# Performance work log

Measured on AMD Instinct MI355X. Metric: run time of the kernel, lower is better.

## Reference

```python
import jax, jax.numpy as jnp
import numpy as np

B, S, HD, NH, AH, F = 64, 256, 512, 8, 256, 2
DH = HD // NH          # item/pos head dim = 64
DA = AH // NH          # attribute head dim = 32
EPS = 1e-12


def setup_inputs() -> dict:
    key = jax.random.key(0)
    ks = iter(jax.random.split(key, 32))
    rn = lambda shape, s=1.0: jax.random.normal(next(ks), shape, dtype=jnp.float32) * s
    w = 0.02
    return {
        "input_tensor": rn((B, S, HD)),
        "attribute_table": rn((B, S, 1, AH)),
        "position_embedding": rn((B, S, HD)),
        "Wq": rn((HD, HD), w), "bq": jnp.zeros((HD,), jnp.float32),
        "Wk": rn((HD, HD), w), "bk": jnp.zeros((HD,), jnp.float32),
        "Wv": rn((HD, HD), w), "bv": jnp.zeros((HD,), jnp.float32),
        "Wqp": rn((HD, HD), w), "bqp": jnp.zeros((HD,), jnp.float32),
        "Wkp": rn((HD, HD), w), "bkp": jnp.zeros((HD,), jnp.float32),
        "Wqa": rn((F, AH, AH), w), "bqa": jnp.zeros((F, AH), jnp.float32),
        "Wka": rn((F, AH, AH), w), "bka": jnp.zeros((F, AH), jnp.float32),
        "fw1": rn((S, S), w), "fb1": jnp.zeros((S,), jnp.float32),
        "fw2": rn((1, S), w), "fb2": jnp.zeros((1,), jnp.float32),
        "Wd": rn((HD, HD), w), "bd": jnp.zeros((HD,), jnp.float32),
        "gamma": jnp.ones((HD,), jnp.float32),
        "beta": jnp.zeros((HD,), jnp.float32),
    }


def _split_heads(x, nh):
    b, s, h = x.shape
    return x.reshape(b, s, nh, h // nh).transpose(0, 2, 1, 3)  # [B,H,S,d]


def reference(input_tensor, attribute_table, position_embedding,
              Wq, bq, Wk, bk, Wv, bv, Wqp, bqp, Wkp, bkp,
              Wqa, bqa, Wka, bka, fw1, fb1, fw2, fb2,
              Wd, bd, gamma, beta):
    q = _split_heads(input_tensor @ Wq.T + bq, NH)
    k = _split_heads(input_tensor @ Wk.T + bk, NH)
    v = _split_heads(input_tensor @ Wv.T + bv, NH)
    qp = _split_heads(position_embedding @ Wqp.T + bqp, NH)
    kp = _split_heads(position_embedding @ Wkp.T + bkp, NH)

    item_scores = jnp.einsum('bhqd,bhkd->bhqk', q, k)
    pos_scores = jnp.einsum('bhqd,bhkd->bhqk', qp, kp)

    attr = attribute_table.squeeze(-2)                       # [B,S,AH]
    qa = jnp.einsum('bsc,foc->fbso', attr, Wqa) + bqa[:, None, None, :]
    ka = jnp.einsum('bsc,foc->fbso', attr, Wka) + bka[:, None, None, :]
    qa = qa.reshape(F, B, S, NH, DA).transpose(0, 1, 3, 2, 4)  # [F,B,H,S,da]
    ka = ka.reshape(F, B, S, NH, DA).transpose(0, 1, 3, 2, 4)
    attr_scores = jnp.einsum('fbhqd,fbhkd->fbhqk', qa, ka)
    attr_scores = attr_scores.transpose(1, 2, 3, 0, 4)         # [B,H,S,F,S]

    # gate fusion (VanillaAttention over the F+2 score sources)
    stacked = jnp.concatenate(
        [attr_scores, item_scores[..., None, :], pos_scores[..., None, :]],
        axis=-2)                                               # [B,H,S,F+2,S]
    energy = jnp.maximum(stacked @ fw1.T + fb1, 0.0) @ fw2.T + fb2
    gate_w = jax.nn.softmax(energy.squeeze(-1), axis=-1)        # [B,H,S,F+2]
    scores = jnp.sum(stacked * gate_w[..., None], axis=-2)      # [B,H,S,S]

    scores = scores / np.sqrt(DH).astype(np.float32)
    probs = jax.nn.softmax(scores, axis=-1)
    ctx = jnp.einsum('bhqk,bhkd->bhqd', probs, v)
    ctx = ctx.transpose(0, 2, 1, 3).reshape(B, S, HD)

    h = ctx @ Wd.T + bd
    x = h + input_tensor
    mu = jnp.mean(x, axis=-1, keepdims=True)
    var = jnp.mean(jnp.square(x - mu), axis=-1, keepdims=True)
    return gamma * (x - mu) / jnp.sqrt(var + EPS) + beta
```

## Files before the change

kernel.cpp:

```cpp
#include <hip/hip_runtime.h>

typedef unsigned short u16;
typedef unsigned int   u32;
typedef __bf16 bf16x8 __attribute__((ext_vector_type(8)));
typedef float  f32x4  __attribute__((ext_vector_type(4)));
typedef u16    u16x4  __attribute__((ext_vector_type(4)));
typedef u16    u16x8  __attribute__((ext_vector_type(8)));

#define BB 64
#define SS 256
#define HDIM 512
#define NHEAD 8
#define BS (BB*SS)
#define NBH 512

__device__ __forceinline__ u16 f2bf(float f){
    u32 u = __builtin_bit_cast(u32, f);
    u32 r = u + 0x7FFFu + ((u>>16)&1u);
    return (u16)(r>>16);
}
__device__ __forceinline__ float bf2f(u16 u){
    return __builtin_bit_cast(float, (u32)u<<16);
}
__device__ __forceinline__ void gload16(const void* g, void* l){
    __builtin_amdgcn_global_load_lds(
        (const __attribute__((address_space(1))) void*)g,
        (__attribute__((address_space(3))) void*)l, 16, 0, 0);
}

__device__ __forceinline__ size_t zrow(int bh, int s){
    return ((size_t)bh*256 + s)*384;
}

__global__ __launch_bounds__(256) void cvt_k(const float* __restrict__ s,
                                             u16* __restrict__ d, int n8)
{
    int i = blockIdx.x*256 + threadIdx.x;
    const int stride = gridDim.x*256;
    for (; i < n8; i += stride) {
        f32x4 a = ((const f32x4*)s)[i*2];
        f32x4 b = ((const f32x4*)s)[i*2+1];
        u16x8 o = { f2bf(a[0]),f2bf(a[1]),f2bf(a[2]),f2bf(a[3]),
                    f2bf(b[0]),f2bf(b[1]),f2bf(b[2]),f2bf(b[3]) };
        ((u16x8*)d)[i] = o;
    }
}

__global__ __launch_bounds__(256) void cvtW_k(
    const float* __restrict__ Wq,  const float* __restrict__ Wk,
    const float* __restrict__ Wv,  const float* __restrict__ Wqp,
    const float* __restrict__ Wkp, const float* __restrict__ Wqa,
    const float* __restrict__ Wka, const float* __restrict__ Wd,
    u16* __restrict__ dst)
{
    const int i = blockIdx.x*256 + threadIdx.x;
    const float* s; u16* d; int local;
    if (i < 163840) {
        const int seg = i >> 15; local = i & 32767;
        s = seg==0?Wq:seg==1?Wk:seg==2?Wv:seg==3?Wqp:Wkp;
        d = dst + (size_t)seg*262144;
    } else if (i < 196608) {
        const int j = i - 163840; const int seg = j >> 14; local = j & 16383;
        s = seg ? Wka : Wqa;
        d = dst + 1310720 + (size_t)seg*131072;
    } else {
        local = i - 196608;
        s = Wd; d = dst + 1572864;
    }
    f32x4 a = ((const f32x4*)s)[local*2];
    f32x4 b = ((const f32x4*)s)[local*2+1];
    u16x8 o = { f2bf(a[0]),f2bf(a[1]),f2bf(a[2]),f2bf(a[3]),
                f2bf(b[0]),f2bf(b[1]),f2bf(b[2]),f2bf(b[3]) };
    ((u16x8*)d)[local] = o;
}

__global__ __launch_bounds__(64) void prep_fw1(const float* __restrict__ fw1,
                                               u16* __restrict__ fw1b)
{
    const int row = blockIdx.x;
    const int c0  = threadIdx.x * 4;
    float4 v = *(const float4*)(fw1 + (size_t)row*256 + c0);
    u16x4 pk = { f2bf(v.x), f2bf(v.y), f2bf(v.z), f2bf(v.w) };
    *(u16x4*)((char*)fw1b + (size_t)row*512 + ((c0*2) ^ ((row&7)<<4))) = pk;
}

template<int OUTMODE, int BBF16>
__global__ __launch_bounds__(256,2) void gemm128(
    const u16* __restrict__ A, const void* __restrict__ Bv,
    void* __restrict__ o0, void* __restrict__ o1, void* __restrict__ o2,
    const float* __restrict__ b0, const float* __restrict__ b1,
    const float* __restrict__ b2, const float* __restrict__ resid,
    int N, int K)
{
    __shared__ char sA[16384];
    __shared__ char sB[16384];
    const int tid = threadIdx.x, lane = tid & 63, w = tid >> 6;
    const int wr = (w & 1) * 64, wc = (w >> 1) * 64;
    const int flat = blockIdx.x;
    const int xcd = flat & 7, bi2 = flat >> 3;
    const int n_i = bi2 >> 4, mIn = bi2 & 15;
    const int m0 = (xcd*16 + mIn)*128, n0 = n_i*128;

    f32x4 acc[4][4];
    #pragma unroll
    for (int mi = 0; mi < 4; mi++)
        #pragma unroll
        for (int ni = 0; ni < 4; ni++) acc[mi][ni] = (f32x4){0.f,0.f,0.f,0.f};

    for (int k0 = 0; k0 < K; k0 += 64) {
        __syncthreads();
        #pragma unroll
        for (int i = 0; i < 4; i++) {
            const int off = w*4096 + i*1024 + lane*16;
            const int r = off >> 7, c = off & 0x70;
            gload16(A + (size_t)(m0 + r)*K + k0 + ((c ^ ((r&7)<<4)) >> 1),
                    sA + w*4096 + i*1024);
        }
        if (BBF16) {
            const u16* B = (const u16*)Bv;
            #pragma unroll
            for (int i = 0; i < 4; i++) {
                const int off = w*4096 + i*1024 + lane*16;
                const int r = off >> 7, c = off & 0x70;
                gload16(B + (size_t)(n0 + r)*K + k0 + ((c ^ ((r&7)<<4)) >> 1),
                        sB + w*4096 + i*1024);
            }
        } else {
            const float* B = (const float*)Bv;
            const int r = tid >> 1, cseg = (tid & 1) * 32;
            const float* p = B + (size_t)(n0 + r)*K + k0 + cseg;
            alignas(16) u16 tmp[32];
            #pragma unroll
            for (int j = 0; j < 8; j++) {
                float4 fv = ((const float4*)p)[j];
                tmp[j*4+0]=f2bf(fv.x); tmp[j*4+1]=f2bf(fv.y);
                tmp[j*4+2]=f2bf(fv.z); tmp[j*4+3]=f2bf(fv.w);
            }
            const int rx = (r&7)<<4;
            #pragma unroll
            for (int j = 0; j < 4; j++)
                *(u16x8*)(sB + r*128 + ((cseg*2 + j*16) ^ rx)) = *(u16x8*)(tmp + j*8);
        }
        __syncthreads();
        bf16x8 af[2][4], bf[2][4];
        #pragma unroll
        for (int ks = 0; ks < 2; ks++) {
            const int kb = ks*64 + (lane>>4)*16;
            #pragma unroll
            for (int mi = 0; mi < 4; mi++) {
                const int r = wr + mi*16 + (lane&15);
                af[ks][mi] = *(const bf16x8*)(sA + r*128 + (kb ^ ((r&7)<<4)));
            }
            #pragma unroll
            for (int ni = 0; ni < 4; ni++) {
                const int r = wc + ni*16 + (lane&15);
                bf[ks][ni] = *(const bf16x8*)(sB + r*128 + (kb ^ ((r&7)<<4)));
            }
        }
        #pragma unroll
        for (int ks = 0; ks < 2; ks++)
            #pragma unroll
            for (int mi = 0; mi < 4; mi++)
                #pragma unroll
                for (int ni = 0; ni < 4; ni++)
                    acc[mi][ni] = __builtin_amdgcn_mfma_f32_16x16x32_bf16(
                        af[ks][mi], bf[ks][ni], acc[mi][ni], 0,0,0);
    }
    #pragma unroll
    for (int mi = 0; mi < 4; mi++) {
        const int rowb = m0 + wr + mi*16 + (lane>>4)*4;
        const int bi = rowb >> 8, s0 = rowb & 255;
        #pragma unroll
        for (int ni = 0; ni < 4; ni++) {
            const int gn = n0 + wc + ni*16 + (lane&15);
            if (OUTMODE == 2) {
                float* out = (float*)o0;
                const float bb = b0[gn];
                #pragma unroll
                for (int r = 0; r < 4; r++) {
                    size_t idx = (size_t)(rowb+r)*N + gn;
                    out[idx] = acc[mi][ni][r] + bb + resid[idx];
                }
            } else if (OUTMODE == 4) {
                const int seg = gn >> 9, o = gn & 511;
                const int hh = o >> 6, d = o & 63;
                const float bb = (seg==0?b0:seg==1?b1:b2)[o];
                const int bh = bi*8 + hh;
                if (seg < 2) {
                    char* outp = (char*)(seg ? o1 : o0);
                    #pragma unroll
                    for (int r = 0; r < 4; r++) {
                        const int s = s0 + r;
                        *(u16*)(outp + zrow(bh,s) + ((d*2) ^ ((s&7)<<4)))
                            = f2bf(acc[mi][ni][r] + bb);
                    }
                } else {
                    u16x4 pk;
                    #pragma unroll
                    for (int r = 0; r < 4; r++) pk[r] = f2bf(acc[mi][ni][r] + bb);
                    *(u16x4*)((char*)o2 + (size_t)bh*32768 + d*512
                                        + ((s0*2) ^ ((d&7)<<4))) = pk;
                }
            } else if (OUTMODE == 5) {
                const int seg = gn >> 9, o = gn & 511;
                const int hh = o >> 6, d = o & 63;
                const float bb = (seg ? b1 : b0)[o];
                const int bh = bi*8 + hh;
                char* outp = (char*)(seg ? o1 : o0);
                #pragma unroll
                for (int r = 0; r < 4; r++) {
                    const int s = s0 + r;
                    *(u16*)(outp + zrow(bh,s) + (((64+d)*2) ^ ((s&7)<<4)))
                        = f2bf(acc[mi][ni][r] + bb);
                }
            } else {
                const int qk = gn >> 9, fo = gn & 511;
                const int f = fo >> 8, o = fo & 255;
                const int hh = o >> 5, d = o & 31;
                const int cb = 128 + f*32;
                const float bb = (qk ? b1 : b0)[fo];
                const int bh = bi*8 + hh;
                char* outp = (char*)(qk ? o1 : o0);
                #pragma unroll
                for (int r = 0; r < 4; r++) {
                    const int s = s0 + r;
                    *(u16*)(outp + zrow(bh,s) + (((cb+d)*2) ^ ((s&7)<<4)))
                        = f2bf(acc[mi][ni][r] + bb);
                }
            }
        }
    }
}

#define K34B_QZ   53248
#define K34B_QZSZ 13312
#define K34B_SMEM (53248 + 2*13312)

__global__ __launch_bounds__(512,4) void k34b(
    const u16* __restrict__ QZ, const u16* __restrict__ KZ,
    const u16* __restrict__ fw1b, const float* __restrict__ fb1,
    const float* __restrict__ fw2, float* __restrict__ e)
{
    extern __shared__ char sm[];
    const int tid = threadIdx.x, lane = tid & 63, w = tid >> 6;
    const int bh = blockIdx.x >> 1, sp = blockIdx.x & 1;
    const int l15 = lane & 15, lq = lane >> 4;
    const int base0 = sp ? 64 : 0;
    const int base1 = sp ? 160 : 128;

    auto stage_qz = [&](int qt4, int buf) {
        char* dst = sm + K34B_QZ + buf*K34B_QZSZ;
        {
            const int li = w*64 + lane;
            const int q = li / 13, c = li - q*13;
            const int cc = (c == 12) ? 0 : c;
            const int ld = cc*8;
            const int gd = (ld < 64) ? base0 + ld : base1 + (ld - 64);
            gload16((const char*)QZ + zrow(bh, qt4*64 + q)
                        + ((gd*2) ^ ((q&7)<<4)),
                    dst + w*1024);
        }
        if (w < 5) {
            const int li = 512 + w*64 + lane;
            const int q = li / 13, c = li - q*13;
            const int cc = (c == 12) ? 0 : c;
            const int ld = cc*8;
            const int gd = (ld < 64) ? base0 + ld : base1 + (ld - 64);
            gload16((const char*)QZ + zrow(bh, qt4*64 + q)
                        + ((gd*2) ^ ((q&7)<<4)),
                    dst + 8192 + w*1024);
        }
    };

    stage_qz(0, 0);
    {
        const int spair = tid & 127, dg = tid >> 7;
        const int s0 = spair*2;
        const char* r0 = (const char*)KZ + zrow(bh, s0);
        const char* r1 = (const char*)KZ + zrow(bh, s0+1);
        const int sw0 = (s0&7)<<4, sw1 = ((s0+1)&7)<<4;
        #pragma unroll
        for (int m = 0; m < 3; m++) {
            const int ld0 = dg*24 + m*8;
            const int gd = (ld0 < 64) ? base0 + ld0 : base1 + (ld0 - 64);
            u16x8 v0 = *(const u16x8*)(r0 + ((gd*2) ^ sw0));
            u16x8 v1 = *(const u16x8*)(r1 + ((gd*2) ^ sw1));
            #pragma unroll
            for (int ee = 0; ee < 8; ee++) {
                const int d = ld0 + ee;
                *(u32*)(sm + d*512 + ((s0*2) ^ ((d&7)<<4)))
                    = (u32)v0[ee] | ((u32)v1[ee] << 16);
            }
        }
    }
    __syncthreads();

    const int jb = w & 3, dh = w >> 2;
    f32x4 kacc[4][3];
    #pragma unroll
    for (int js = 0; js < 4; js++)
        #pragma unroll
        for (int ni = 0; ni < 3; ni++) kacc[js][ni] = (f32x4){0.f,0.f,0.f,0.f};
    #pragma unroll
    for (int ks = 0; ks < 8; ks++) {
        const int kb = ks*64 + lq*16;
        bf16x8 a[4];
        #pragma unroll
        for (int js = 0; js < 4; js++) {
            const int ar = jb*64 + js*16 + l15;
            a[js] = *(const bf16x8*)((const char*)fw1b + (size_t)ar*512
                                     + (kb ^ ((l15&7)<<4)));
        }
        #pragma unroll
        for (int ni = 0; ni < 3; ni++) {
            const int dr = dh*48 + ni*16 + l15;
            bf16x8 b = *(const bf16x8*)(sm + dr*512 + (kb ^ ((dr&7)<<4)));
            #pragma unroll
            for (int js = 0; js < 4; js++)
                kacc[js][ni] = __builtin_amdgcn_mfma_f32_16x16x32_bf16(
                    a[js], b, kacc[js][ni], 0,0,0);
        }
    }
    __syncthreads();

    #pragma unroll
    for (int js = 0; js < 4; js++)
        #pragma unroll
        for (int ni = 0; ni < 3; ni++) {
            const int d = dh*48 + ni*16 + l15;
            #pragma unroll
            for (int r = 0; r < 4; r++) {
                const int j = jb*64 + js*16 + lq*4 + r;
                *(u16*)(sm + j*208 + d*2) = f2bf(kacc[js][ni][r]);
            }
        }
    __syncthreads();

    const int qh = w >> 2;
    bf16x8 af2[4][3];
    #pragma unroll
    for (int js = 0; js < 4; js++) {
        const int ar = jb*64 + js*16 + l15;
        #pragma unroll
        for (int ks = 0; ks < 3; ks++)
            af2[js][ks] = *(const bf16x8*)(sm + ar*208 + ks*64 + lq*16);
    }
    float f1v[4][4], f2v[4][4];
    #pragma unroll
    for (int js = 0; js < 4; js++)
        #pragma unroll
        for (int r = 0; r < 4; r++) {
            const int j = jb*64 + js*16 + lq*4 + r;
            f1v[js][r] = fb1[j]; f2v[js][r] = fw2[j];
        }

    for (int qt = 0; qt < 4; qt++) {
        __syncthreads();
        if (qt < 3) stage_qz(qt+1, (qt+1)&1);
        const char* qb = sm + K34B_QZ + (qt&1)*K34B_QZSZ;
        #pragma unroll
        for (int qs = 0; qs < 2; qs++) {
            const int qoff = (qh*32 + qs*16 + l15)*208 + lq*16;
            f32x4 acc[4];
            #pragma unroll
            for (int js = 0; js < 4; js++) acc[js] = (f32x4){0.f,0.f,0.f,0.f};
            #pragma unroll
            for (int kk = 0; kk < 2; kk++) {
                bf16x8 b = *(const bf16x8*)(qb + qoff + kk*64);
                #pragma unroll
                for (int js = 0; js < 4; js++)
                    acc[js] = __builtin_amdgcn_mfma_f32_16x16x32_bf16(
                        af2[js][kk], b, acc[js], 0,0,0);
            }
            {
                float ep = 0.f;
                #pragma unroll
                for (int js = 0; js < 4; js++)
                    #pragma unroll
                    for (int r = 0; r < 4; r++)
                        ep += fmaxf(acc[js][r] + f1v[js][r], 0.f) * f2v[js][r];
                ep += __shfl_xor(ep, 16);
                ep += __shfl_xor(ep, 32);
                if (lane < 16)
                    ((float*)sm)[(jb*2 + 0)*256 + qt*64 + qh*32 + qs*16 + lane] = ep;
            }
            #pragma unroll
            for (int js = 0; js < 4; js++) acc[js] = (f32x4){0.f,0.f,0.f,0.f};
            {
                bf16x8 b = *(const bf16x8*)(qb + qoff + 128);
                #pragma unroll
                for (int js = 0; js < 4; js++)
                    acc[js] = __builtin_amdgcn_mfma_f32_16x16x32_bf16(
                        af2[js][2], b, acc[js], 0,0,0);
            }
            {
                float ep = 0.f;
                #pragma unroll
                for (int js = 0; js < 4; js++)
                    #pragma unroll
                    for (int r = 0; r < 4; r++)
                        ep += fmaxf(acc[js][r] + f1v[js][r], 0.f) * f2v[js][r];
                ep += __shfl_xor(ep, 16);
                ep += __shfl_xor(ep, 32);
                if (lane < 16)
                    ((float*)sm)[(jb*2 + 1)*256 + qt*64 + qh*32 + qs*16 + lane] = ep;
            }
        }
    }
    __syncthreads();
    {
        const int q = tid & 255, sl = tid >> 8;
        const float* el = (const float*)sm;
        float s = 0.f;
        #pragma unroll
        for (int j2 = 0; j2 < 4; j2++) s += el[(j2*2 + sl)*256 + q];
        const int gsrc = sl ? (2 + sp) : sp;
        e[((size_t)bh*256 + q)*4 + gsrc] = s;
    }
}

#define K5_KZ 24576
#define K5_VT 49152
#define K5_SMEM 81920

__global__ __launch_bounds__(256,2) void k5_mix(
    const u16* __restrict__ QZ, const u16* __restrict__ KZ,
    const u16* __restrict__ VT, const float* __restrict__ e,
    u16* __restrict__ ctx)
{
    extern __shared__ char sm[];
    const int tid = threadIdx.x, lane = tid & 63, w = tid >> 6;
    const int flat = blockIdx.x;
    const int xcd = flat & 7, idx = flat >> 3;
    const int qt = idx & 3;
    const int bh = (idx >> 2) * 8 + xcd;
    const int q0 = qt*64;
    const int b = bh >> 3, h = bh & 7;
    const int kq16 = (lane>>4)*16;

    #pragma unroll
    for (int i = 0; i < 6; i++)
        gload16((const char*)QZ + zrow(bh, q0) + i*4096 + w*1024 + lane*16,
                sm + i*4096 + w*1024);
    #pragma unroll
    for (int i = 0; i < 8; i++)
        gload16((const char*)VT + (size_t)bh*32768 + i*4096 + w*1024 + lane*16,
                sm + K5_VT + i*4096 + w*1024);
    #pragma unroll
    for (int i = 0; i < 6; i++)
        gload16((const char*)KZ + zrow(bh, 0) + i*4096 + w*1024 + lane*16,
                sm + K5_KZ + i*4096 + w*1024);
    __syncthreads();

    const int qrow = w*16 + (lane&15);
    float ga[4];
    {
        f32x4 ev = *(const f32x4*)(e + ((size_t)bh*256 + q0 + qrow)*4);
        float em = fmaxf(fmaxf(ev[0],ev[1]), fmaxf(ev[2],ev[3]));
        float s = 0.f;
        #pragma unroll
        for (int j = 0; j < 4; j++) { ga[j] = __expf(ev[j]-em); s += ga[j]; }
        const float gi = 1.f / s;
        #pragma unroll
        for (int j = 0; j < 4; j++) ga[j] *= gi;
    }
    const int asw = ((lane&15)&7) << 4;
    bf16x8 aF[6];
    #pragma unroll
    for (int ks = 0; ks < 6; ks++) {
        const int sidx = (ks<2)?0:(ks<4)?1:(ks<5)?2:3;
        u16x8 v = *(const u16x8*)(sm + qrow*384 + ((ks*64 + kq16) ^ asw));
        const float gg = ga[sidx];
        u16x8 pk;
        #pragma unroll
        for (int j = 0; j < 8; j++) pk[j] = f2bf(bf2f(v[j]) * gg);
        aF[ks] = __builtin_bit_cast(bf16x8, pk);
    }

    f32x4 macc[4][4];
    #pragma unroll
    for (int kt = 0; kt < 4; kt++)
        #pragma unroll
        for (int n = 0; n < 4; n++) macc[kt][n] = (f32x4){0.f,0.f,0.f,0.f};
    u16x8 kreg[6];
    #pragma unroll
    for (int kt = 0; kt < 4; kt++) {
        if (kt < 3) {
            #pragma unroll
            for (int j = 0; j < 6; j++)
                kreg[j] = *(const u16x8*)((const char*)KZ + zrow(bh, (kt+1)*64)
                                          + (tid + j*256)*16);
        }
        #pragma unroll
        for (int n = 0; n < 4; n++) {
            const int kr = n*16 + (lane&15);
            const int ksw = (kr&7)<<4;
            #pragma unroll
            for (int ks = 0; ks < 6; ks++) {
                bf16x8 bb = *(const bf16x8*)(sm + K5_KZ + kr*384 + ((ks*64 + kq16) ^ ksw));
                macc[kt][n] = __builtin_amdgcn_mfma_f32_16x16x32_bf16(
                    aF[ks], bb, macc[kt][n], 0,0,0);
            }
        }
        if (kt < 3) {
            __syncthreads();
            #pragma unroll
            for (int j = 0; j < 6; j++)
                *(u16x8*)(sm + K5_KZ + (tid + j*256)*16) = kreg[j];
            __syncthreads();
        }
    }
    __syncthreads();

    #pragma unroll
    for (int rr = 0; rr < 4; rr++) {
        float mx = -3.4e38f;
        #pragma unroll
        for (int kt = 0; kt < 4; kt++)
            #pragma unroll
            for (int n = 0; n < 4; n++) mx = fmaxf(mx, macc[kt][n][rr]);
        #pragma unroll
        for (int msk = 1; msk < 16; msk <<= 1) mx = fmaxf(mx, __shfl_xor(mx, msk));
        float s = 0.f;
        #pragma unroll
        for (int kt = 0; kt < 4; kt++)
            #pragma unroll
            for (int n = 0; n < 4; n++) {
                float pv = __expf((macc[kt][n][rr] - mx) * 0.125f);
                macc[kt][n][rr] = pv; s += pv;
            }
        #pragma unroll
        for (int msk = 1; msk < 16; msk <<= 1) s += __shfl_xor(s, msk);
        const float inv = 1.f / s;
        const int orow = w*16 + (lane>>4)*4 + rr;
        const int osw = (orow&7)<<4;
        #pragma unroll
        for (int kt = 0; kt < 4; kt++)
            #pragma unroll
            for (int n = 0; n < 4; n++) {
                const int col = kt*64 + n*16 + (lane&15);
                *(u16*)(sm + orow*512 + ((col*2) ^ osw)) = f2bf(macc[kt][n][rr]*inv);
            }
    }
    __syncthreads();

    f32x4 pacc[4];
    #pragma unroll
    for (int n = 0; n < 4; n++) pacc[n] = (f32x4){0.f,0.f,0.f,0.f};
    const int prow = w*16 + (lane&15);
    const int psw = ((lane&15)&7)<<4;
    #pragma unroll
    for (int ks = 0; ks < 8; ks++) {
        const int kb = ks*64 + kq16;
        bf16x8 a = *(const bf16x8*)(sm + prow*512 + (kb ^ psw));
        #pragma unroll
        for (int n = 0; n < 4; n++) {
            const int dr = n*16 + (lane&15);
            bf16x8 bb = *(const bf16x8*)(sm + K5_VT + dr*512 + (kb ^ ((dr&7)<<4)));
            pacc[n] = __builtin_amdgcn_mfma_f32_16x16x32_bf16(a, bb, pacc[n], 0,0,0);
        }
    }
    {
        const int orow = w*16 + (lane>>4)*4;
        #pragma unroll
        for (int n = 0; n < 4; n++) {
            const int d = n*16 + (lane&15);
            #pragma unroll
            for (int r = 0; r < 4; r++) {
                const size_t grow = (size_t)b*256 + q0 + orow + r;
                ctx[grow*512 + h*64 + d] = f2bf(pacc[n][r]);
            }
        }
    }
}

__global__ __launch_bounds__(256) void ln_k(float* __restrict__ x,
    const float* __restrict__ gamma, const float* __restrict__ beta)
{
    const int row = blockIdx.x*4 + (threadIdx.x >> 6);
    const int l = threadIdx.x & 63;
    float* p = x + (size_t)row*HDIM;
    f32x4 v0 = *(const f32x4*)(p + l*4);
    f32x4 v1 = *(const f32x4*)(p + 256 + l*4);
    float s = v0[0]+v0[1]+v0[2]+v0[3] + v1[0]+v1[1]+v1[2]+v1[3];
    #pragma unroll
    for (int msk = 1; msk < 64; msk <<= 1) s += __shfl_xor(s, msk);
    const float mu = s * (1.f/512.f);
    float vs = 0.f;
    #pragma unroll
    for (int j = 0; j < 4; j++) {
        float d0 = v0[j]-mu, d1 = v1[j]-mu;
        vs += d0*d0 + d1*d1;
    }
    #pragma unroll
    for (int msk = 1; msk < 64; msk <<= 1) vs += __shfl_xor(vs, msk);
    const float inv = 1.f / sqrtf(vs * (1.f/512.f) + 1e-12f);
    f32x4 o0, o1;
    #pragma unroll
    for (int j = 0; j < 4; j++) {
        o0[j] = gamma[l*4+j]     * (v0[j]-mu) * inv + beta[l*4+j];
        o1[j] = gamma[256+l*4+j] * (v1[j]-mu) * inv + beta[256+l*4+j];
    }
    *(f32x4*)(p + l*4) = o0;
    *(f32x4*)(p + 256 + l*4) = o1;
}

extern "C" void kernel_launch(void* const* d_in, const int* in_sizes, int n_in,
                              void* d_out, int out_size, void* d_ws, size_t ws_size,
                              hipStream_t stream)
{
    const float* input = (const float*)d_in[0];
    const float* attrt = (const float*)d_in[1];
    const float* pose  = (const float*)d_in[2];
    const float* Wq  = (const float*)d_in[3];  const float* bq  = (const float*)d_in[4];
    const float* Wk  = (const float*)d_in[5];  const float* bk  = (const float*)d_in[6];
    const float* Wv  = (const float*)d_in[7];  const float* bv  = (const float*)d_in[8];
    const float* Wqp = (const float*)d_in[9];  const float* bqp = (const float*)d_in[10];
    const float* Wkp = (const float*)d_in[11]; const float* bkp = (const float*)d_in[12];
    const float* Wqa = (const float*)d_in[13]; const float* bqa = (const float*)d_in[14];
    const float* Wka = (const float*)d_in[15]; const float* bka = (const float*)d_in[16];
    const float* fw1 = (const float*)d_in[17]; const float* fb1 = (const float*)d_in[18];
    const float* fw2 = (const float*)d_in[19];
    const float* Wd  = (const float*)d_in[21]; const float* bd  = (const float*)d_in[22];
    const float* gamma = (const float*)d_in[23]; const float* beta = (const float*)d_in[24];

    char* ws = (char*)d_ws;
    u16*   wsQZ  = (u16*)(ws);
    u16*   wsKZ  = (u16*)(ws + 50331648);
    u16*   wsTmp = (u16*)(ws + 100663296);
    float* wsE   = (float*)(ws + 117440512);
    u16*   fw1b  = (u16*)(ws + 119537664);
    u16*   dW    = (u16*)(ws + 119668736);
    u16*   wsVT  = (u16*)d_out;

    dim3 blk(256);

    cvtW_k<<<dim3(896), blk, 0, stream>>>(Wq, Wk, Wv, Wqp, Wkp, Wqa, Wka, Wd, dW);
    prep_fw1<<<dim3(256), dim3(64), 0, stream>>>(fw1, fw1b);

    cvt_k<<<dim3(2048), blk, 0, stream>>>(attrt, wsTmp, 524288);
    gemm128<6,1><<<dim3(1024), blk, 0, stream>>>(wsTmp, dW + 1310720,
        wsQZ, wsKZ, nullptr, bqa, bka, nullptr, nullptr, 1024, 256);
    cvt_k<<<dim3(2048), blk, 0, stream>>>(input, wsTmp, 1048576);
    gemm128<4,1><<<dim3(1536), blk, 0, stream>>>(wsTmp, dW,
        wsQZ, wsKZ, wsVT, bq, bk, bv, nullptr, 1536, 512);
    cvt_k<<<dim3(2048), blk, 0, stream>>>(pose, wsTmp, 1048576);
    gemm128<5,1><<<dim3(1024), blk, 0, stream>>>(wsTmp, dW + 786432,
        wsQZ, wsKZ, nullptr, bqp, bkp, nullptr, nullptr, 1024, 512);

    hipFuncSetAttribute(reinterpret_cast<const void*>(k34b),
                        hipFuncAttributeMaxDynamicSharedMemorySize, K34B_SMEM);
    k34b<<<dim3(NBH*2), dim3(512), K34B_SMEM, stream>>>(wsQZ, wsKZ, fw1b, fb1, fw2, wsE);

    hipFuncSetAttribute(reinterpret_cast<const void*>(k5_mix),
                        hipFuncAttributeMaxDynamicSharedMemorySize, K5_SMEM);
    k5_mix<<<dim3(2048), blk, K5_SMEM, stream>>>(wsQZ, wsKZ, wsVT, wsE, wsTmp);

    gemm128<2,1><<<dim3(512), blk, 0, stream>>>(wsTmp, dW + 1572864,
        d_out, nullptr, nullptr, bd, nullptr, nullptr, input, 512, 512);
    ln_k<<<dim3(BS/4), blk, 0, stream>>>((float*)d_out, gamma, beta);
}
```

Before: 238.5 us.

## Split gate-energy kernel into three 64-dim chunks per head to cut shared memory

The gate-energy kernel is restructured from two blocks per (batch, head), each handling 96 feature dims, to three blocks per head, each handling a contiguous 64-dim chunk of the Z rows selected by blockIdx.y. The intermediate K·fw1 tile shrinks to 128-byte swizzled rows, Q staging becomes a simple 8-loads-per-row copy, and shared memory drops to 48 KB with launch bounds raised from 4 to 6 blocks per CU. The aim is higher occupancy and simpler, conflict-free LDS access. The cost is that the fw1 projection of K is now recomputed for three chunks instead of two, and the tail chunk branches on sc to produce two separate energies.

```diff
diff --git a/kernel.cpp b/kernel.cpp
--- a/kernel.cpp
+++ b/kernel.cpp
@@ -232,59 +232,37 @@
     }
 }
 
-#define K34B_QZ   53248
-#define K34B_QZSZ 13312
-#define K34B_SMEM (53248 + 2*13312)
-
-__global__ __launch_bounds__(512,4) void k34b(
+#define K34C_QZ   32768
+#define K34C_QZSZ 8192
+#define K34C_SMEM 49152
+
+__global__ __launch_bounds__(512,6) void k34c(
     const u16* __restrict__ QZ, const u16* __restrict__ KZ,
     const u16* __restrict__ fw1b, const float* __restrict__ fb1,
     const float* __restrict__ fw2, float* __restrict__ e)
 {
     extern __shared__ char sm[];
     const int tid = threadIdx.x, lane = tid & 63, w = tid >> 6;
-    const int bh = blockIdx.x >> 1, sp = blockIdx.x & 1;
+    const int bh = blockIdx.x, sc = blockIdx.y;
     const int l15 = lane & 15, lq = lane >> 4;
-    const int base0 = sp ? 64 : 0;
-    const int base1 = sp ? 160 : 128;
-
-    auto stage_qz = [&](int qt4, int buf) {
-        char* dst = sm + K34B_QZ + buf*K34B_QZSZ;
-        {
-            const int li = w*64 + lane;
-            const int q = li / 13, c = li - q*13;
-            const int cc = (c == 12) ? 0 : c;
-            const int ld = cc*8;
-            const int gd = (ld < 64) ? base0 + ld : base1 + (ld - 64);
-            gload16((const char*)QZ + zrow(bh, qt4*64 + q)
-                        + ((gd*2) ^ ((q&7)<<4)),
-                    dst + w*1024);
-        }
-        if (w < 5) {
-            const int li = 512 + w*64 + lane;
-            const int q = li / 13, c = li - q*13;
-            const int cc = (c == 12) ? 0 : c;
-            const int ld = cc*8;
-            const int gd = (ld < 64) ? base0 + ld : base1 + (ld - 64);
-            gload16((const char*)QZ + zrow(bh, qt4*64 + q)
-                        + ((gd*2) ^ ((q&7)<<4)),
-                    dst + 8192 + w*1024);
-        }
-    };
-
-    stage_qz(0, 0);
+    const int gdoff = sc * 128;
+
     {
-        const int spair = tid & 127, dg = tid >> 7;
-        const int s0 = spair*2;
-        const char* r0 = (const char*)KZ + zrow(bh, s0);
-        const char* r1 = (const char*)KZ + zrow(bh, s0+1);
+        const int q = tid >> 3, c = tid & 7;
+        gload16((const char*)QZ + zrow(bh, q) + gdoff + c*16,
+                sm + K34C_QZ + tid*16);
+    }
+    {
+        const int sp = tid & 127, dg = tid >> 7;
+        const int s0 = sp*2;
+        const char* r0 = (const char*)KZ + zrow(bh, s0)   + gdoff;
+        const char* r1 = (const char*)KZ + zrow(bh, s0+1) + gdoff;
         const int sw0 = (s0&7)<<4, sw1 = ((s0+1)&7)<<4;
         #pragma unroll
-        for (int m = 0; m < 3; m++) {
-            const int ld0 = dg*24 + m*8;
-            const int gd = (ld0 < 64) ? base0 + ld0 : base1 + (ld0 - 64);
-            u16x8 v0 = *(const u16x8*)(r0 + ((gd*2) ^ sw0));
-            u16x8 v1 = *(const u16x8*)(r1 + ((gd*2) ^ sw1));
+        for (int m = 0; m < 2; m++) {
+            const int ld0 = dg*16 + m*8;
+            u16x8 v0 = *(const u16x8*)(r0 + ((ld0*2) ^ sw0));
+            u16x8 v1 = *(const u16x8*)(r1 + ((ld0*2) ^ sw1));
             #pragma unroll
             for (int ee = 0; ee < 8; ee++) {
                 const int d = ld0 + ee;
@@ -295,28 +273,27 @@
     }
     __syncthreads();
 
-    const int jb = w & 3, dh = w >> 2;
-    f32x4 kacc[4][3];
-    #pragma unroll
-    for (int js = 0; js < 4; js++)
-        #pragma unroll
-        for (int ni = 0; ni < 3; ni++) kacc[js][ni] = (f32x4){0.f,0.f,0.f,0.f};
+    f32x4 kacc[2][4];
+    #pragma unroll
+    for (int js = 0; js < 2; js++)
+        #pragma unroll
+        for (int ni = 0; ni < 4; ni++) kacc[js][ni] = (f32x4){0.f,0.f,0.f,0.f};
     #pragma unroll
     for (int ks = 0; ks < 8; ks++) {
         const int kb = ks*64 + lq*16;
-        bf16x8 a[4];
-        #pragma unroll
-        for (int js = 0; js < 4; js++) {
-            const int ar = jb*64 + js*16 + l15;
+        bf16x8 a[2];
+        #pragma unroll
+        for (int js = 0; js < 2; js++) {
+            const int ar = w*32 + js*16 + l15;
             a[js] = *(const bf16x8*)((const char*)fw1b + (size_t)ar*512
                                      + (kb ^ ((l15&7)<<4)));
         }
         #pragma unroll
-        for (int ni = 0; ni < 3; ni++) {
-            const int dr = dh*48 + ni*16 + l15;
+        for (int ni = 0; ni < 4; ni++) {
+            const int dr = ni*16 + l15;
             bf16x8 b = *(const bf16x8*)(sm + dr*512 + (kb ^ ((dr&7)<<4)));
             #pragma unroll
-            for (int js = 0; js < 4; js++)
+            for (int js = 0; js < 2; js++)
                 kacc[js][ni] = __builtin_amdgcn_mfma_f32_16x16x32_bf16(
                     a[js], b, kacc[js][ni], 0,0,0);
         }
@@ -324,55 +301,62 @@
     __syncthreads();
 
     #pragma unroll
-    for (int js = 0; js < 4; js++)
-        #pragma unroll
-        for (int ni = 0; ni < 3; ni++) {
-            const int d = dh*48 + ni*16 + l15;
+    for (int js = 0; js < 2; js++)
+        #pragma unroll
+        for (int ni = 0; ni < 4; ni++) {
+            const int d = ni*16 + l15;
             #pragma unroll
             for (int r = 0; r < 4; r++) {
-                const int j = jb*64 + js*16 + lq*4 + r;
-                *(u16*)(sm + j*208 + d*2) = f2bf(kacc[js][ni][r]);
-            }
-        }
-    __syncthreads();
-
-    const int qh = w >> 2;
-    bf16x8 af2[4][3];
+                const int j = w*32 + js*16 + lq*4 + r;
+                *(u16*)(sm + j*128 + ((d*2) ^ ((j&7)<<4))) = f2bf(kacc[js][ni][r]);
+            }
+        }
+    __syncthreads();
+
+    const int jb = w & 3, qh = w >> 2;
+    bf16x8 af2[4][2];
     #pragma unroll
     for (int js = 0; js < 4; js++) {
         const int ar = jb*64 + js*16 + l15;
-        #pragma unroll
-        for (int ks = 0; ks < 3; ks++)
-            af2[js][ks] = *(const bf16x8*)(sm + ar*208 + ks*64 + lq*16);
-    }
-    float f1v[4][4], f2v[4][4];
-    #pragma unroll
-    for (int js = 0; js < 4; js++)
-        #pragma unroll
-        for (int r = 0; r < 4; r++) {
-            const int j = jb*64 + js*16 + lq*4 + r;
-            f1v[js][r] = fb1[j]; f2v[js][r] = fw2[j];
-        }
+        const int asw = (ar&7)<<4;
+        #pragma unroll
+        for (int kk = 0; kk < 2; kk++)
+            af2[js][kk] = *(const bf16x8*)(sm + ar*128 + ((kk*64 + lq*16) ^ asw));
+    }
+    f32x4 f1v[4], f2v[4];
+    #pragma unroll
+    for (int js = 0; js < 4; js++) {
+        const int j = jb*64 + js*16 + lq*4;
+        f1v[js] = *(const f32x4*)(fb1 + j);
+        f2v[js] = *(const f32x4*)(fw2 + j);
+    }
+    __syncthreads();
 
     for (int qt = 0; qt < 4; qt++) {
-        __syncthreads();
-        if (qt < 3) stage_qz(qt+1, (qt+1)&1);
-        const char* qb = sm + K34B_QZ + (qt&1)*K34B_QZSZ;
+        if (qt < 3) {
+            const int q = tid >> 3, c = tid & 7;
+            gload16((const char*)QZ + zrow(bh, (qt+1)*64 + q) + gdoff + c*16,
+                    sm + K34C_QZ + ((qt+1)&1)*K34C_QZSZ + tid*16);
+        }
+        const char* qb = sm + K34C_QZ + (qt&1)*K34C_QZSZ;
         #pragma unroll
         for (int qs = 0; qs < 2; qs++) {
-            const int qoff = (qh*32 + qs*16 + l15)*208 + lq*16;
+            const int qrow = qh*32 + qs*16 + l15;
+            const int qsw = (qrow&7)<<4;
+            bf16x8 b0 = *(const bf16x8*)(qb + qrow*128 + ((lq*16) ^ qsw));
+            bf16x8 b1 = *(const bf16x8*)(qb + qrow*128 + ((64 + lq*16) ^ qsw));
             f32x4 acc[4];
-            #pragma unroll
-            for (int js = 0; js < 4; js++) acc[js] = (f32x4){0.f,0.f,0.f,0.f};
-            #pragma unroll
-            for (int kk = 0; kk < 2; kk++) {
-                bf16x8 b = *(const bf16x8*)(qb + qoff + kk*64);
+            if (sc < 2) {
+                #pragma unroll
+                for (int js = 0; js < 4; js++) acc[js] = (f32x4){0.f,0.f,0.f,0.f};
                 #pragma unroll
                 for (int js = 0; js < 4; js++)
                     acc[js] = __builtin_amdgcn_mfma_f32_16x16x32_bf16(
-                        af2[js][kk], b, acc[js], 0,0,0);
-            }
-            {
+                        af2[js][0], b0, acc[js], 0,0,0);
+                #pragma unroll
+                for (int js = 0; js < 4; js++)
+                    acc[js] = __builtin_amdgcn_mfma_f32_16x16x32_bf16(
+                        af2[js][1], b1, acc[js], 0,0,0);
                 float ep = 0.f;
                 #pragma unroll
                 for (int js = 0; js < 4; js++)
@@ -383,18 +367,30 @@
                 ep += __shfl_xor(ep, 32);
                 if (lane < 16)
                     ((float*)sm)[(jb*2 + 0)*256 + qt*64 + qh*32 + qs*16 + lane] = ep;
-            }
-            #pragma unroll
-            for (int js = 0; js < 4; js++) acc[js] = (f32x4){0.f,0.f,0.f,0.f};
-            {
-                bf16x8 b = *(const bf16x8*)(qb + qoff + 128);
+            } else {
+                #pragma unroll
+                for (int js = 0; js < 4; js++) acc[js] = (f32x4){0.f,0.f,0.f,0.f};
                 #pragma unroll
                 for (int js = 0; js < 4; js++)
                     acc[js] = __builtin_amdgcn_mfma_f32_16x16x32_bf16(
-                        af2[js][2], b, acc[js], 0,0,0);
-            }
-            {
+                        af2[js][0], b0, acc[js], 0,0,0);
                 float ep = 0.f;
+                #pragma unroll
+                for (int js = 0; js < 4; js++)
+                    #pragma unroll
+                    for (int r = 0; r < 4; r++)
+                        ep += fmaxf(acc[js][r] + f1v[js][r], 0.f) * f2v[js][r];
+                ep += __shfl_xor(ep, 16);
+                ep += __shfl_xor(ep, 32);
+                if (lane < 16)
+                    ((float*)sm)[(jb*2 + 0)*256 + qt*64 + qh*32 + qs*16 + lane] = ep;
+                #pragma unroll
+                for (int js = 0; js < 4; js++) acc[js] = (f32x4){0.f,0.f,0.f,0.f};
+                #pragma unroll
+                for (int js = 0; js < 4; js++)
+                    acc[js] = __builtin_amdgcn_mfma_f32_16x16x32_bf16(
+                        af2[js][1], b1, acc[js], 0,0,0);
+                ep = 0.f;
                 #pragma unroll
                 for (int js = 0; js < 4; js++)
                     #pragma unroll
@@ -406,16 +402,19 @@
                     ((float*)sm)[(jb*2 + 1)*256 + qt*64 + qh*32 + qs*16 + lane] = ep;
             }
         }
+        if (qt < 3) __syncthreads();
     }
     __syncthreads();
     {
         const int q = tid & 255, sl = tid >> 8;
         const float* el = (const float*)sm;
-        float s = 0.f;
-        #pragma unroll
-        for (int j2 = 0; j2 < 4; j2++) s += el[(j2*2 + sl)*256 + q];
-        const int gsrc = sl ? (2 + sp) : sp;
-        e[((size_t)bh*256 + q)*4 + gsrc] = s;
+        if (sc == 2 || sl == 0) {
+            float s = 0.f;
+            #pragma unroll
+            for (int j2 = 0; j2 < 4; j2++) s += el[(j2*2 + sl)*256 + q];
+            const int gsrc = (sc == 2) ? (2 + sl) : sc;
+            e[((size_t)bh*256 + q)*4 + gsrc] = s;
+        }
     }
 }
 
@@ -648,9 +647,9 @@
     gemm128<5,1><<<dim3(1024), blk, 0, stream>>>(wsTmp, dW + 786432,
         wsQZ, wsKZ, nullptr, bqp, bkp, nullptr, nullptr, 1024, 512);
 
-    hipFuncSetAttribute(reinterpret_cast<const void*>(k34b),
-                        hipFuncAttributeMaxDynamicSharedMemorySize, K34B_SMEM);
-    k34b<<<dim3(NBH*2), dim3(512), K34B_SMEM, stream>>>(wsQZ, wsKZ, fw1b, fb1, fw2, wsE);
+    hipFuncSetAttribute(reinterpret_cast<const void*>(k34c),
+                        hipFuncAttributeMaxDynamicSharedMemorySize, K34C_SMEM);
+    k34c<<<dim3(NBH, 3), dim3(512), K34C_SMEM, stream>>>(wsQZ, wsKZ, fw1b, fb1, fw2, wsE);
 
     hipFuncSetAttribute(reinterpret_cast<const void*>(k5_mix),
                         hipFuncAttributeMaxDynamicSharedMemorySize, K5_SMEM);
```

New measurement: 296.9 us. 24.5% more time.
